# Kernel tuning notes

Measured on AMD Instinct MI355X. Metric: run time of the kernel, lower is better.

Reference implementation:

```python
import jax, jax.numpy as jnp
import numpy as np

B, T = 128, 256
H = 200                      # hidden_dim
EMB, POSD, NERD = 300, 30, 30
VOCAB, NPOS, NNER = 40000, 50, 25
NCLASS = 2
IN = EMB + POSD + NERD


def setup_inputs():
    key = jax.random.key(0)
    ks = jax.random.split(key, 32)
    words = jax.random.randint(ks[0], (B, T), 1, VOCAB)
    lengths = jax.random.randint(ks[1], (B,), T // 2, T + 1)
    t = jnp.arange(T)
    masks = (t[None, :] >= lengths[:, None]).astype(jnp.int64)  # 1 = pad
    pos = jax.random.randint(ks[2], (B, T), 0, NPOS)
    ner = jax.random.randint(ks[3], (B, T), 0, NNER)

    def span_pos(k, span):  # relative position encoding, 0 on entity span
        start = jax.random.randint(k, (B,), 0, T // 2 - span)
        rel = t[None, :] - start[:, None]
        return jnp.where(rel < 0, rel, jnp.where(rel < span, 0, rel - span + 1)).astype(jnp.int64)

    subj_pos = span_pos(ks[4], 3)
    obj_pos = span_pos(ks[5], 2)

    s = 0.08
    def rn(k, shape):
        return jax.random.normal(k, shape, dtype=jnp.float32) * s

    p = {}
    p["emb_w"] = rn(ks[6], (VOCAB, EMB)).at[0].set(0.0)  # PAD row
    p["pos_w"] = rn(ks[7], (NPOS, POSD))
    p["ner_w"] = rn(ks[8], (NNER, NERD))
    dims = [IN, 2 * H]
    i = 9
    for l in range(2):
        for d in ("f", "b"):
            p["w_ih_l%d%s" % (l, d)] = rn(ks[i], (4 * H, dims[l])); i += 1
            p["w_hh_l%d%s" % (l, d)] = rn(ks[i], (4 * H, H)); i += 1
            p["b_l%d%s" % (l, d)] = rn(ks[i], (4 * H,)); i += 1
    p["wo_w"] = rn(ks[i], (H, 2 * H)); p["wo_b"] = rn(ks[i + 1], (H,))
    p["ws_w"] = rn(ks[i + 2], (H, 2 * H)); p["ws_b"] = rn(ks[i + 3], (H,))
    p["wg_w"] = rn(ks[i + 4], (H, 2 * H)); p["wg_b"] = rn(ks[i + 5], (H,))
    p["cls_w"] = rn(ks[i + 6], (NCLASS, H)); p["cls_b"] = rn(ks[i + 7], (NCLASS,))
    return dict(words=words, masks=masks, pos=pos, ner=ner,
                subj_pos=subj_pos, obj_pos=obj_pos, **p)


def lstm_dir(x, keep, w_ih, w_hh, b, reverse):
    """Packed-sequence-equivalent LSTM: state frozen and output zeroed at pads.
    x: [B,T,D], keep: [B,T] (1.0 = real token). Returns ([B,T,H], final h [B,H])."""
    Hh = w_hh.shape[1]

    def step(carry, inp):
        h, c = carry
        xt, mt = inp  # [B,D], [B,1]
        g = xt @ w_ih.T + h @ w_hh.T + b
        i, f, gg, o = jnp.split(g, 4, axis=-1)  # torch gate order i,f,g,o
        cn = jax.nn.sigmoid(f) * c + jax.nn.sigmoid(i) * jnp.tanh(gg)
        hn = jax.nn.sigmoid(o) * jnp.tanh(cn)
        h = mt * hn + (1.0 - mt) * h
        c = mt * cn + (1.0 - mt) * c
        return (h, c), h * mt

    b_ = x.shape[0]
    h0 = jnp.zeros((b_, Hh), x.dtype)
    xs = (jnp.swapaxes(x, 0, 1), keep.T[..., None])
    (hT, _), ys = jax.lax.scan(step, (h0, h0), xs, reverse=reverse)
    return jnp.swapaxes(ys, 0, 1), hT


def attn_pool(q, kv, pad):
    # single-query attention: q [B,D], kv [B,T,D], pad [B,T] bool
    d_k = q.shape[-1]
    scores = jnp.einsum("bd,btd->bt", q, kv) / jnp.sqrt(jnp.float32(d_k))
    scores = jnp.where(pad, jnp.float32(-1e9), scores)
    p = jax.nn.softmax(scores, axis=-1)
    return jnp.einsum("bt,btd->bd", p, kv)


def _forward(words, masks, pos, ner, subj_pos, obj_pos,
             emb_w, pos_w, ner_w,
             w_ih_l0f, w_hh_l0f, b_l0f, w_ih_l0b, w_hh_l0b, b_l0b,
             w_ih_l1f, w_hh_l1f, b_l1f, w_ih_l1b, w_hh_l1b, b_l1b,
             wo_w, wo_b, ws_w, ws_b, wg_w, wg_b, cls_w, cls_b):
    embs = jnp.concatenate([emb_w[words], pos_w[pos], ner_w[ner]], axis=-1)
    keep = (masks == 0).astype(embs.dtype)
    of0, _ = lstm_dir(embs, keep, w_ih_l0f, w_hh_l0f, b_l0f, False)
    ob0, _ = lstm_dir(embs, keep, w_ih_l0b, w_hh_l0b, b_l0b, True)
    x1 = jnp.concatenate([of0, ob0], axis=-1)
    of1, hf1 = lstm_dir(x1, keep, w_ih_l1f, w_hh_l1f, b_l1f, False)
    ob1, hb1 = lstm_dir(x1, keep, w_ih_l1b, w_hh_l1b, b_l1b, True)
    rnn_out = jnp.concatenate([of1, ob1], axis=-1)  # [B,T,2H]

    pad = masks != 0
    # masked gather-sum over entity spans: (rel_pos + mask) == 0 selects span tokens
    subj_sel = ((subj_pos + masks) == 0).astype(rnn_out.dtype)[..., None]
    obj_sel = ((obj_pos + masks) == 0).astype(rnn_out.dtype)[..., None]
    subj_h = jnp.sum(rnn_out * subj_sel, axis=1)  # [B,2H]
    obj_h = jnp.sum(rnn_out * obj_sel, axis=1)
    glob_h = jnp.concatenate([hb1, hf1], axis=-1)  # hidden[-1]=last bwd, hidden[-2]=last fwd

    obj_a = attn_pool(obj_h, rnn_out, pad)
    subj_a = attn_pool(subj_h, rnn_out, pad)
    glob_a = attn_pool(glob_h, rnn_out, pad)

    h = jax.nn.relu(obj_a @ wo_w.T + wo_b + subj_a @ ws_w.T + ws_b + glob_a @ wg_w.T + wg_b)
    return h @ cls_w.T + cls_b  # [B, NCLASS]


def reference(words, masks, pos, ner, subj_pos, obj_pos,
              emb_w, pos_w, ner_w,
              w_ih_l0f, w_hh_l0f, b_l0f, w_ih_l0b, w_hh_l0b, b_l0b,
              w_ih_l1f, w_hh_l1f, b_l1f, w_ih_l1b, w_hh_l1b, b_l1b,
              wo_w, wo_b, ws_w, ws_b, wg_w, wg_b, cls_w, cls_b):
    return _forward(words, masks, pos, ner, subj_pos, obj_pos,
                    emb_w, pos_w, ner_w,
                    w_ih_l0f, w_hh_l0f, b_l0f, w_ih_l0b, w_hh_l0b, b_l0b,
                    w_ih_l1f, w_hh_l1f, b_l1f, w_ih_l1b, w_hh_l1b, b_l1b,
                    wo_w, wo_b, ws_w, ws_b, wg_w, wg_b, cls_w, cls_b)
```

## Files before the change

kernel.cpp:

```cpp
#include <hip/hip_runtime.h>
#include <hip/hip_bf16.h>
#include <math.h>

constexpr int B = 128;
constexpr int T = 256;
constexpr int H = 200;
constexpr int G4 = 800;
constexpr int BT = B * T;
constexpr int K0 = 360, K0P = 384;
constexpr int K1 = 400, K1P = 416;

typedef __bf16 bf16x8 __attribute__((ext_vector_type(8)));
typedef float f32x4 __attribute__((ext_vector_type(4)));
typedef _Float16 half2v __attribute__((ext_vector_type(2)));
typedef unsigned uix4 __attribute__((ext_vector_type(4)));

__device__ __forceinline__ float bfr2f(unsigned short u) {
  union { unsigned int i; float f; } x;
  x.i = ((unsigned int)u) << 16;
  return x.f;
}
__device__ __forceinline__ unsigned short f2hu(float f) {
  _Float16 h = (_Float16)f;
  return *(unsigned short*)&h;
}
__device__ __forceinline__ half2v ash2(unsigned u) {
  union { unsigned v; half2v h; } x;
  x.v = u;
  return x.h;
}
__device__ __forceinline__ float sigm(float x) {
  return 1.0f / (1.0f + __expf(-x));
}
__device__ __forceinline__ float tanh_f(float x) {
  float e = __expf(2.0f * x);
  return (e - 1.0f) / (e + 1.0f);
}
__device__ __forceinline__ float ldraw(const void* p, size_t i, int f) {
  return f ? ((const float*)p)[i] : bfr2f(((const unsigned short*)p)[i]);
}

__global__ void detect_dtype(const unsigned short* __restrict__ raw,
                             int* __restrict__ flag) {
  __shared__ int cnt[256];
  int c = 0;
  for (int j = 0; j < 32; ++j) {
    unsigned short u = raw[1024 + threadIdx.x * 32 + j];
    int e = (u >> 7) & 0xFF;
    if (e >= 0xC0) ++c;
  }
  cnt[threadIdx.x] = c;
  __syncthreads();
  for (int off = 128; off > 0; off >>= 1) {
    if (threadIdx.x < off) cnt[threadIdx.x] += cnt[threadIdx.x + off];
    __syncthreads();
  }
  if (threadIdx.x == 0) *flag = (cnt[0] > 16) ? 1 : 0;
}

__global__ __launch_bounds__(256) void embed_fill(
    const int* __restrict__ words,
    const int* __restrict__ pos,
    const int* __restrict__ ner,
    const void* __restrict__ emb_w,
    const void* __restrict__ pos_w,
    const void* __restrict__ ner_w,
    __hip_bfloat16* __restrict__ X0,
    uix4* __restrict__ z0, size_t n0,
    uix4* __restrict__ z1, size_t n1,
    const int* __restrict__ flag) {
  if (blockIdx.x < 4096) {
    int bt = blockIdx.x * 8 + (threadIdx.x >> 5);
    int j0 = threadIdx.x & 31;
    int f = *flag;
    int w = words[bt], p = pos[bt], nr = ner[bt];
    for (int j = j0; j < K0P; j += 32) {
      float v;
      if (j < 300)       v = ldraw(emb_w, (size_t)w * 300 + j, f);
      else if (j < 330)  v = ldraw(pos_w, (size_t)p * 30 + (j - 300), f);
      else if (j < 360)  v = ldraw(ner_w, (size_t)nr * 30 + (j - 330), f);
      else               v = 0.0f;
      X0[(size_t)bt * K0P + j] = __float2bfloat16(v);
    }
  } else {
    size_t i = (size_t)(blockIdx.x - 4096) * 256 + threadIdx.x;
    size_t stride = (size_t)2048 * 256;
    uix4 z = {0u, 0u, 0u, 0u};
    size_t nt = n0 + n1;
    for (; i < nt; i += stride) {
      if (i < n0) z0[i] = z;
      else        z1[i - n0] = z;
    }
  }
}

__global__ __launch_bounds__(256) void prep_weights(
    const void* __restrict__ whh0, const void* __restrict__ whh1,
    const void* __restrict__ whh2, const void* __restrict__ whh3,
    unsigned* __restrict__ wpack,
    const void* __restrict__ wih0f, const void* __restrict__ wih0b,
    __hip_bfloat16* __restrict__ wih0p,
    const void* __restrict__ wih1f, const void* __restrict__ wih1b,
    __hip_bfloat16* __restrict__ wih1p,
    const int* __restrict__ flag) {
  int blk = blockIdx.x;
  int f = *flag;
  if (blk < 1250) {
    int idx = blk * 256 + threadIdx.x;
    if (idx >= 4 * G4 * 100) return;
    int m = idx / (G4 * 100);
    int loc = idx - m * (G4 * 100);
    const void* src = (m == 0) ? whh0 : (m == 1) ? whh1 : (m == 2) ? whh2 : whh3;
    int n = loc / 100, p = loc - n * 100;
    float lo_f = ldraw(src, (size_t)n * 200 + 2 * p, f);
    float hi_f = ldraw(src, (size_t)n * 200 + 2 * p + 1, f);
    wpack[idx] = (unsigned)f2hu(lo_f) | ((unsigned)f2hu(hi_f) << 16);
  } else if (blk < 2850) {
    int r = blk - 1250;
    const void* src = (r < G4) ? wih0f : wih0b;
    int rr = (r < G4) ? r : r - G4;
    for (int j = threadIdx.x; j < K0P; j += 256) {
      float v = (j < K0) ? ldraw(src, (size_t)rr * K0 + j, f) : 0.0f;
      wih0p[(size_t)r * K0P + j] = __float2bfloat16(v);
    }
  } else {
    int r = blk - 2850;
    const void* src = (r < G4) ? wih1f : wih1b;
    int rr = (r < G4) ? r : r - G4;
    for (int j = threadIdx.x; j < K1P; j += 256) {
      float v = (j < K1) ? ldraw(src, (size_t)rr * K1 + j, f) : 0.0f;
      wih1p[(size_t)r * K1P + j] = __float2bfloat16(v);
    }
  }
}

__global__ __launch_bounds__(256) void gemm_bt(
    const __hip_bfloat16* __restrict__ A,
    const __hip_bfloat16* __restrict__ Bm,
    __hip_bfloat16* __restrict__ C,
    int N, int Kp) {
  const int tid = threadIdx.x;
  const int lane = tid & 63;
  const int wave = tid >> 6;
  const int l15 = lane & 15, quad = lane >> 4;
  const int wr = wave & 1, wc = wave >> 1;

  const int blk = blockIdx.x;
  const int x = blk & 7, j = blk >> 3;
  const int m0 = (x + 8 * (j / 13)) * 128;
  const int n0 = (j % 13) * 128;

  __shared__ __align__(16) __hip_bfloat16 Ab[2][128 * 64];
  __shared__ __align__(16) __hip_bfloat16 Bb[2][128 * 64];

  f32x4 acc[4][4] = {};

  const int nk = (Kp + 63) >> 6;

  uix4 st[8];
  auto stage_issue = [&](int kt) {
    const int k0 = kt << 6;
    #pragma unroll
    for (int jj = 0; jj < 8; ++jj) {
      int c = tid + (jj & 3) * 256;
      int row = c >> 3, p = c & 7;
      int qd = p ^ (row & 7);
      int kcol = k0 + qd * 8;
      uix4 z = {0u, 0u, 0u, 0u};
      if (kcol + 8 <= Kp) {
        if (jj < 4) {
          st[jj] = *(const uix4*)(A + (size_t)(m0 + row) * Kp + kcol);
        } else {
          int br = n0 + row; if (br > N - 1) br = N - 1;
          st[jj] = *(const uix4*)(Bm + (size_t)br * Kp + kcol);
        }
      } else {
        st[jj] = z;
      }
    }
  };
  auto stage_write = [&](int buf) {
    #pragma unroll
    for (int jj = 0; jj < 8; ++jj) {
      int c = tid + (jj & 3) * 256;
      if (jj < 4) *(uix4*)((char*)&Ab[buf][0] + c * 16) = st[jj];
      else        *(uix4*)((char*)&Bb[buf][0] + c * 16) = st[jj];
    }
  };

  stage_issue(0);
  stage_write(0);
  __syncthreads();

  for (int kt = 0; kt < nk; ++kt) {
    const int buf = kt & 1;
    if (kt + 1 < nk) stage_issue(kt + 1);

    #pragma unroll
    for (int k32 = 0; k32 < 2; ++k32) {
      bf16x8 a[4], b[4];
      #pragma unroll
      for (int mi = 0; mi < 4; ++mi) {
        int row = wr * 64 + mi * 16 + l15;
        int p = (k32 * 4 + quad) ^ (row & 7);
        a[mi] = *(const bf16x8*)((const char*)&Ab[buf][0] + (row * 8 + p) * 16);
      }
      #pragma unroll
      for (int ni = 0; ni < 4; ++ni) {
        int row = wc * 64 + ni * 16 + l15;
        int p = (k32 * 4 + quad) ^ (row & 7);
        b[ni] = *(const bf16x8*)((const char*)&Bb[buf][0] + (row * 8 + p) * 16);
      }
      #pragma unroll
      for (int mi = 0; mi < 4; ++mi)
        #pragma unroll
        for (int ni = 0; ni < 4; ++ni)
          acc[mi][ni] = __builtin_amdgcn_mfma_f32_16x16x32_bf16(
              a[mi], b[ni], acc[mi][ni], 0, 0, 0);
    }

    if (kt + 1 < nk) stage_write((kt + 1) & 1);
    __syncthreads();
  }

  #pragma unroll
  for (int mi = 0; mi < 4; ++mi)
    #pragma unroll
    for (int ni = 0; ni < 4; ++ni)
      #pragma unroll
      for (int r = 0; r < 4; ++r) {
        int row = m0 + wr * 64 + mi * 16 + quad * 4 + r;
        int col = n0 + wc * 64 + ni * 16 + l15;
        if (col < N)
          C[(size_t)row * N + col] = __float2bfloat16(acc[mi][ni][r]);
      }
}

__global__ __launch_bounds__(512, 2) void lstm_row(
    const __hip_bfloat16* __restrict__ Gpre,
    const unsigned* __restrict__ Wpack,
    const void* __restrict__ bias_f_raw,
    const void* __restrict__ bias_b_raw,
    const int* __restrict__ masks,
    __hip_bfloat16* __restrict__ out,
    int ostride,
    float* __restrict__ final_h,
    const int* __restrict__ flag)
{
  const int tid = threadIdx.x;
  const int dir = blockIdx.x >> 7;
  const int row = blockIdx.x & 127;
  const int wave = tid >> 6;
  const int lane = tid & 63;
  const int kq = wave & 3;
  const int gs = ((wave >> 2) << 6) | lane;
  const bool tail = (gs >= 96);

  __shared__ __align__(16) _Float16 hsh[256];
  __shared__ float parts[4 * 804];
  __shared__ int lensh[256];
  __shared__ int bigbuf[21504];

  const unsigned* wb = Wpack + (size_t)dir * G4 * 100;

  for (int i = tid; i < 3200; i += 512) {
    int g = i / 100, c = i - g * 100;
    bigbuf[g * 101 + c] = (int)wb[(768 + g) * 100 + c];
  }
  if (tid < 256) lensh[tid] = (masks[row * T + tid] == 0) ? 1 : 0;

  unsigned w[6][25];
  {
    const unsigned* s = wb + gs * 100 + kq * 25;
    #pragma unroll
    for (int j = 0; j < 6; ++j)
      #pragma unroll
      for (int p = 0; p < 25; ++p)
        w[j][p] = s[12800 * j + p];
  }
  const unsigned* wt = (const unsigned*)&bigbuf[(gs - 96) * 101 + kq * 25];

  const int u = tid;
  const int f = *flag;
  const void* braw = dir ? bias_b_raw : bias_f_raw;
  float bI = 0.f, bF = 0.f, bG = 0.f, bO = 0.f;
  if (u < 200) {
    bI = ldraw(braw, u, f);
    bF = ldraw(braw, 200 + u, f);
    bG = ldraw(braw, 400 + u, f);
    bO = ldraw(braw, 600 + u, f);
  }

  if (tid < 256) hsh[tid] = (_Float16)0.0f;
  float creg = 0.0f, hreg = 0.0f;
  __syncthreads();

  for (int off = 128; off > 0; off >>= 1) {
    if (tid < off) lensh[tid] += lensh[tid + off];
    __syncthreads();
  }
  const int len = lensh[0];

  const unsigned short* gp = (const unsigned short*)Gpre + dir * 800;
  const size_t gbase = (size_t)row * T;
  const uix4* hvp = (const uix4*)((const char*)hsh + kq * 128);
  const int hwrite = (u / 50) * 64 + (u % 50);

  #pragma unroll 1
  for (int tt = 0; tt < len; ++tt) {
    const int t = dir ? (len - 1 - tt) : tt;
    const size_t goff = (gbase + t) * 1600;
    unsigned short qI = 0, qF = 0, qG = 0, qO = 0;
    if (u < 200) {
      qI = gp[goff + u];
      qF = gp[goff + 200 + u];
      qG = gp[goff + 400 + u];
      qO = gp[goff + 600 + u];
    }

    uix4 hb[7];
    #pragma unroll
    for (int i = 0; i < 7; ++i) hb[i] = hvp[i];

    float a0 = 0.f, a1 = 0.f, a2 = 0.f, a3 = 0.f, a4 = 0.f, a5 = 0.f;
    #pragma unroll
    for (int p = 0; p < 25; ++p) {
      half2v h2 = ash2(hb[p >> 2][p & 3]);
      a0 = __builtin_amdgcn_fdot2(ash2(w[0][p]), h2, a0, false);
      a1 = __builtin_amdgcn_fdot2(ash2(w[1][p]), h2, a1, false);
      a2 = __builtin_amdgcn_fdot2(ash2(w[2][p]), h2, a2, false);
      a3 = __builtin_amdgcn_fdot2(ash2(w[3][p]), h2, a3, false);
      a4 = __builtin_amdgcn_fdot2(ash2(w[4][p]), h2, a4, false);
      a5 = __builtin_amdgcn_fdot2(ash2(w[5][p]), h2, a5, false);
    }
    const int pb = kq * 804;
    parts[pb + gs]        = a0;
    parts[pb + 128 + gs]  = a1;
    parts[pb + 256 + gs]  = a2;
    parts[pb + 384 + gs]  = a3;
    parts[pb + 512 + gs]  = a4;
    parts[pb + 640 + gs]  = a5;
    if (tail) {
      float a6 = 0.f;
      #pragma unroll
      for (int p = 0; p < 25; ++p)
        a6 = __builtin_amdgcn_fdot2(ash2(wt[p]), ash2(hb[p >> 2][p & 3]), a6, false);
      parts[pb + 672 + gs] = a6;
    }
    __syncthreads();

    if (u < 200) {
      float gi = parts[u]       + parts[804 + u]       + parts[1608 + u]       + parts[2412 + u]       + bI + bfr2f(qI);
      float gf = parts[200 + u] + parts[804 + 200 + u] + parts[1608 + 200 + u] + parts[2412 + 200 + u] + bF + bfr2f(qF);
      float gg = parts[400 + u] + parts[804 + 400 + u] + parts[1608 + 400 + u] + parts[2412 + 400 + u] + bG + bfr2f(qG);
      float go = parts[600 + u] + parts[804 + 600 + u] + parts[1608 + 600 + u] + parts[2412 + 600 + u] + bO + bfr2f(qO);
      float si = sigm(gi), sf = sigm(gf), so = sigm(go);
      float cn = sf * creg + si * tanh_f(gg);
      float hn = so * tanh_f(cn);
      creg = cn;
      hreg = hn;
      hsh[hwrite] = (_Float16)hn;
      out[((size_t)row * T + t) * ostride + dir * H + u] = __float2bfloat16(hn);
    }
    __syncthreads();
  }

  if (final_h != nullptr && u < 200) {
    int col = dir ? u : (H + u);
    final_h[(size_t)row * 400 + col] = hreg;
  }
}

__global__ __launch_bounds__(256) void span_sum(
    const __hip_bfloat16* __restrict__ rnn,
    const int* __restrict__ masks,
    const int* __restrict__ subj_pos,
    const int* __restrict__ obj_pos,
    float* __restrict__ obj_h,
    float* __restrict__ subj_h)
{
  int b = blockIdx.x;
  int tc = threadIdx.x >> 6;
  int dv = threadIdx.x & 63;
  __shared__ float aS[4][400];
  __shared__ float aO[4][400];

  float ss[8] = {}, so[8] = {};
  if (dv < 50) {
    for (int t = tc * 64; t < tc * 64 + 64; ++t) {
      int m = masks[b * T + t];
      int fs = (subj_pos[b * T + t] + m) == 0;
      int fo = (obj_pos[b * T + t] + m) == 0;
      if (fs | fo) {
        uix4 v = *(const uix4*)(rnn + ((size_t)b * T + t) * 400 + dv * 8);
        #pragma unroll
        for (int j = 0; j < 4; ++j) {
          float lo = bfr2f((unsigned short)(v[j] & 0xFFFF));
          float hi = bfr2f((unsigned short)(v[j] >> 16));
          if (fs) { ss[2 * j] += lo; ss[2 * j + 1] += hi; }
          if (fo) { so[2 * j] += lo; so[2 * j + 1] += hi; }
        }
      }
    }
    #pragma unroll
    for (int k = 0; k < 8; ++k) {
      aS[tc][dv * 8 + k] = ss[k];
      aO[tc][dv * 8 + k] = so[k];
    }
  }
  __syncthreads();
  for (int d = threadIdx.x; d < 400; d += 256) {
    subj_h[(size_t)b * 400 + d] = aS[0][d] + aS[1][d] + aS[2][d] + aS[3][d];
    obj_h[(size_t)b * 400 + d]  = aO[0][d] + aO[1][d] + aO[2][d] + aO[3][d];
  }
}

__global__ __launch_bounds__(256) void attn_pool_k(
    const float* __restrict__ qbuf,
    const __hip_bfloat16* __restrict__ rnn,
    const int* __restrict__ masks,
    float* __restrict__ outp)
{
  int b = blockIdx.x & 127;
  int qi = blockIdx.x >> 7;
  __shared__ float qs[400];
  __shared__ float ps[256];
  __shared__ float red[256];
  __shared__ float acc4[4][400];
  const float* q = qbuf + ((size_t)qi * B + b) * 400;
  for (int d = threadIdx.x; d < 400; d += 256) qs[d] = q[d];
  __syncthreads();

  int t = threadIdx.x;
  const uix4* kvv = (const uix4*)(rnn + ((size_t)b * T + t) * 400);
  float s = 0.f;
  #pragma unroll 5
  for (int i = 0; i < 50; ++i) {
    uix4 v = kvv[i];
    #pragma unroll
    for (int j = 0; j < 4; ++j) {
      s += bfr2f((unsigned short)(v[j] & 0xFFFF)) * qs[8 * i + 2 * j];
      s += bfr2f((unsigned short)(v[j] >> 16))    * qs[8 * i + 2 * j + 1];
    }
  }
  s *= 0.05f;
  if (masks[b * T + t] != 0) s = -1e9f;

  red[t] = s;
  __syncthreads();
  for (int off = 128; off > 0; off >>= 1) {
    if (t < off) red[t] = fmaxf(red[t], red[t + off]);
    __syncthreads();
  }
  float mx = red[0];
  __syncthreads();
  float e = expf(s - mx);
  red[t] = e;
  __syncthreads();
  for (int off = 128; off > 0; off >>= 1) {
    if (t < off) red[t] += red[t + off];
    __syncthreads();
  }
  float inv = 1.0f / red[0];
  ps[t] = e * inv;
  __syncthreads();

  int tc = threadIdx.x >> 6;
  int dv = threadIdx.x & 63;
  float a[8] = {};
  if (dv < 50) {
    for (int t2 = tc * 64; t2 < tc * 64 + 64; ++t2) {
      float wgt = ps[t2];
      if (wgt != 0.f) {
        uix4 v = *(const uix4*)(rnn + ((size_t)b * T + t2) * 400 + dv * 8);
        #pragma unroll
        for (int j = 0; j < 4; ++j) {
          a[2 * j]     += wgt * bfr2f((unsigned short)(v[j] & 0xFFFF));
          a[2 * j + 1] += wgt * bfr2f((unsigned short)(v[j] >> 16));
        }
      }
    }
    #pragma unroll
    for (int k = 0; k < 8; ++k) acc4[tc][dv * 8 + k] = a[k];
  }
  __syncthreads();
  for (int d = threadIdx.x; d < 400; d += 256)
    outp[((size_t)qi * B + b) * 400 + d] =
        acc4[0][d] + acc4[1][d] + acc4[2][d] + acc4[3][d];
}

__global__ __launch_bounds__(256) void final_head(
    const float* __restrict__ attn,
    const void* __restrict__ wo_w, const void* __restrict__ wo_b,
    const void* __restrict__ ws_w, const void* __restrict__ ws_b,
    const void* __restrict__ wg_w, const void* __restrict__ wg_b,
    const void* __restrict__ cls_w, const void* __restrict__ cls_b,
    void* __restrict__ outp,
    const int* __restrict__ flag)
{
  int b = blockIdx.x;
  int f = *flag;
  __shared__ float hs[H];
  int j = threadIdx.x;
  if (j < H) {
    float acc = ldraw(wo_b, j, f) + ldraw(ws_b, j, f) + ldraw(wg_b, j, f);
    const float* oa = attn + ((size_t)0 * B + b) * 400;
    const float* sa = attn + ((size_t)1 * B + b) * 400;
    const float* ga = attn + ((size_t)2 * B + b) * 400;
    for (int d = 0; d < 400; ++d) {
      acc += oa[d] * ldraw(wo_w, (size_t)j * 400 + d, f);
      acc += sa[d] * ldraw(ws_w, (size_t)j * 400 + d, f);
      acc += ga[d] * ldraw(wg_w, (size_t)j * 400 + d, f);
    }
    hs[j] = fmaxf(acc, 0.0f);
  }
  __syncthreads();
  if (j < 2) {
    float a = ldraw(cls_b, j, f);
    for (int k = 0; k < H; ++k)
      a += hs[k] * ldraw(cls_w, (size_t)j * H + k, f);
    if (f) ((float*)outp)[b * 2 + j] = a;
    else   ((__hip_bfloat16*)outp)[b * 2 + j] = __float2bfloat16(a);
  }
}

constexpr size_t O_X0   = 0;
constexpr size_t O_X1   = 25165824;
constexpr size_t O_GPRE = 52428800;
constexpr size_t O_RNN  = 157286400;
constexpr size_t O_WIH0 = 183500800;
constexpr size_t O_WIH1 = 184729600;
constexpr size_t O_WPK  = 186060800;
constexpr size_t O_Q    = 187340800;
constexpr size_t O_ATT  = 187955200;
constexpr size_t O_FLAG = 188569600;

extern "C" void kernel_launch(void* const* d_in, const int* in_sizes, int n_in,
                              void* d_out, int out_size, void* d_ws, size_t ws_size,
                              hipStream_t stream) {
  (void)in_sizes; (void)n_in; (void)out_size; (void)ws_size;

  const int* words = (const int*)d_in[0];
  const int* masks = (const int*)d_in[1];
  const int* pos   = (const int*)d_in[2];
  const int* ner   = (const int*)d_in[3];
  const int* subj  = (const int*)d_in[4];
  const int* obj   = (const int*)d_in[5];
  const void* emb_w = d_in[6];
  const void* pos_w = d_in[7];
  const void* ner_w = d_in[8];
  const void* wih[4]  = {d_in[9],  d_in[12], d_in[15], d_in[18]};
  const void* whh[4]  = {d_in[10], d_in[13], d_in[16], d_in[19]};
  const void* bias[4] = {d_in[11], d_in[14], d_in[17], d_in[20]};
  const void* wo_w = d_in[21]; const void* wo_b = d_in[22];
  const void* ws_w = d_in[23]; const void* ws_b = d_in[24];
  const void* wg_w = d_in[25]; const void* wg_b = d_in[26];
  const void* cls_w = d_in[27]; const void* cls_b = d_in[28];

  char* ws = (char*)d_ws;
  __hip_bfloat16* X0   = (__hip_bfloat16*)(ws + O_X0);
  __hip_bfloat16* X1   = (__hip_bfloat16*)(ws + O_X1);
  __hip_bfloat16* Gpre = (__hip_bfloat16*)(ws + O_GPRE);
  __hip_bfloat16* RNN  = (__hip_bfloat16*)(ws + O_RNN);
  __hip_bfloat16* wih0p = (__hip_bfloat16*)(ws + O_WIH0);
  __hip_bfloat16* wih1p = (__hip_bfloat16*)(ws + O_WIH1);
  unsigned* Wpack = (unsigned*)(ws + O_WPK);
  float* qbuf = (float*)(ws + O_Q);
  float* attb = (float*)(ws + O_ATT);
  int* flag = (int*)(ws + O_FLAG);

  detect_dtype<<<1, 256, 0, stream>>>((const unsigned short*)emb_w, flag);
  prep_weights<<<4450, 256, 0, stream>>>(
      whh[0], whh[1], whh[2], whh[3], Wpack,
      wih[0], wih[1], wih0p, wih[2], wih[3], wih1p, flag);

  embed_fill<<<6144, 256, 0, stream>>>(words, pos, ner, emb_w, pos_w, ner_w,
                                       X0,
                                       (uix4*)X1, (size_t)BT * K1P * 2 / 16,
                                       (uix4*)RNN, (size_t)BT * 400 * 2 / 16,
                                       flag);

  const int ggrid = (BT / 128) * 13;

  gemm_bt<<<ggrid, 256, 0, stream>>>(X0, wih0p, Gpre, 1600, K0P);
  lstm_row<<<256, 512, 0, stream>>>(Gpre, Wpack, bias[0], bias[1], masks,
                                    X1, K1P, nullptr, flag);

  gemm_bt<<<ggrid, 256, 0, stream>>>(X1, wih1p, Gpre, 1600, K1P);
  float* qglob = qbuf + (size_t)2 * B * 400;
  lstm_row<<<256, 512, 0, stream>>>(Gpre, Wpack + (size_t)2 * G4 * 100,
                                    bias[2], bias[3], masks,
                                    RNN, 400, qglob, flag);

  span_sum<<<B, 256, 0, stream>>>(RNN, masks, subj, obj,
                                  qbuf, qbuf + (size_t)B * 400);

  attn_pool_k<<<3 * B, 256, 0, stream>>>(qbuf, RNN, masks, attb);

  final_head<<<B, 256, 0, stream>>>(attb, wo_w, wo_b, ws_w, ws_b, wg_w, wg_b,
                                    cls_w, cls_b, d_out, flag);
}
```

Before: 1.119 ms.

## Use direct global-to-LDS loads in GEMM and merge prep kernels

The input-projection GEMM now stages full K tiles with global_load_lds instead of loading into registers and then writing LDS. The loop is restructured so the load for tile kt is issued before compute on tile kt-1, with one barrier per iteration, and a register path is kept only for the partial tail tile. The weight-prep and embedding/zero-fill kernels are also merged into one launch to save a kernel launch. Correctness depends on the async LDS writes being complete at the barrier, and the LSTM recurrence, which dominates runtime, is unchanged.

```diff
diff --git a/kernel.cpp b/kernel.cpp
--- a/kernel.cpp
+++ b/kernel.cpp
@@ -38,6 +38,12 @@
 }
 __device__ __forceinline__ float ldraw(const void* p, size_t i, int f) {
   return f ? ((const float*)p)[i] : bfr2f(((const unsigned short*)p)[i]);
+}
+
+__device__ __forceinline__ void glds16(const void* g, void* l) {
+  __builtin_amdgcn_global_load_lds(
+      (const __attribute__((address_space(1))) unsigned int*)g,
+      (__attribute__((address_space(3))) unsigned int*)l, 16, 0, 0);
 }
 
 __global__ void detect_dtype(const unsigned short* __restrict__ raw,
@@ -58,7 +64,14 @@
   if (threadIdx.x == 0) *flag = (cnt[0] > 16) ? 1 : 0;
 }
 
-__global__ __launch_bounds__(256) void embed_fill(
+__global__ __launch_bounds__(256) void prep_all(
+    const void* __restrict__ whh0, const void* __restrict__ whh1,
+    const void* __restrict__ whh2, const void* __restrict__ whh3,
+    unsigned* __restrict__ wpack,
+    const void* __restrict__ wih0f, const void* __restrict__ wih0b,
+    __hip_bfloat16* __restrict__ wih0p,
+    const void* __restrict__ wih1f, const void* __restrict__ wih1b,
+    __hip_bfloat16* __restrict__ wih1p,
     const int* __restrict__ words,
     const int* __restrict__ pos,
     const int* __restrict__ ner,
@@ -68,40 +81,6 @@
     __hip_bfloat16* __restrict__ X0,
     uix4* __restrict__ z0, size_t n0,
     uix4* __restrict__ z1, size_t n1,
-    const int* __restrict__ flag) {
-  if (blockIdx.x < 4096) {
-    int bt = blockIdx.x * 8 + (threadIdx.x >> 5);
-    int j0 = threadIdx.x & 31;
-    int f = *flag;
-    int w = words[bt], p = pos[bt], nr = ner[bt];
-    for (int j = j0; j < K0P; j += 32) {
-      float v;
-      if (j < 300)       v = ldraw(emb_w, (size_t)w * 300 + j, f);
-      else if (j < 330)  v = ldraw(pos_w, (size_t)p * 30 + (j - 300), f);
-      else if (j < 360)  v = ldraw(ner_w, (size_t)nr * 30 + (j - 330), f);
-      else               v = 0.0f;
-      X0[(size_t)bt * K0P + j] = __float2bfloat16(v);
-    }
-  } else {
-    size_t i = (size_t)(blockIdx.x - 4096) * 256 + threadIdx.x;
-    size_t stride = (size_t)2048 * 256;
-    uix4 z = {0u, 0u, 0u, 0u};
-    size_t nt = n0 + n1;
-    for (; i < nt; i += stride) {
-      if (i < n0) z0[i] = z;
-      else        z1[i - n0] = z;
-    }
-  }
-}
-
-__global__ __launch_bounds__(256) void prep_weights(
-    const void* __restrict__ whh0, const void* __restrict__ whh1,
-    const void* __restrict__ whh2, const void* __restrict__ whh3,
-    unsigned* __restrict__ wpack,
-    const void* __restrict__ wih0f, const void* __restrict__ wih0b,
-    __hip_bfloat16* __restrict__ wih0p,
-    const void* __restrict__ wih1f, const void* __restrict__ wih1b,
-    __hip_bfloat16* __restrict__ wih1p,
     const int* __restrict__ flag) {
   int blk = blockIdx.x;
   int f = *flag;
@@ -123,13 +102,34 @@
       float v = (j < K0) ? ldraw(src, (size_t)rr * K0 + j, f) : 0.0f;
       wih0p[(size_t)r * K0P + j] = __float2bfloat16(v);
     }
-  } else {
+  } else if (blk < 4450) {
     int r = blk - 2850;
     const void* src = (r < G4) ? wih1f : wih1b;
     int rr = (r < G4) ? r : r - G4;
     for (int j = threadIdx.x; j < K1P; j += 256) {
       float v = (j < K1) ? ldraw(src, (size_t)rr * K1 + j, f) : 0.0f;
       wih1p[(size_t)r * K1P + j] = __float2bfloat16(v);
+    }
+  } else if (blk < 8546) {
+    int bt = (blk - 4450) * 8 + (threadIdx.x >> 5);
+    int j0 = threadIdx.x & 31;
+    int w = words[bt], p = pos[bt], nr = ner[bt];
+    for (int j = j0; j < K0P; j += 32) {
+      float v;
+      if (j < 300)       v = ldraw(emb_w, (size_t)w * 300 + j, f);
+      else if (j < 330)  v = ldraw(pos_w, (size_t)p * 30 + (j - 300), f);
+      else if (j < 360)  v = ldraw(ner_w, (size_t)nr * 30 + (j - 330), f);
+      else               v = 0.0f;
+      X0[(size_t)bt * K0P + j] = __float2bfloat16(v);
+    }
+  } else {
+    size_t i = (size_t)(blk - 8546) * 256 + threadIdx.x;
+    size_t stride = (size_t)2048 * 256;
+    uix4 z = {0u, 0u, 0u, 0u};
+    size_t nt = n0 + n1;
+    for (; i < nt; i += stride) {
+      if (i < n0) z0[i] = z;
+      else        z1[i - n0] = z;
     }
   }
 }
@@ -155,71 +155,74 @@
 
   f32x4 acc[4][4] = {};
 
-  const int nk = (Kp + 63) >> 6;
-
-  uix4 st[8];
-  auto stage_issue = [&](int kt) {
-    const int k0 = kt << 6;
-    #pragma unroll
-    for (int jj = 0; jj < 8; ++jj) {
-      int c = tid + (jj & 3) * 256;
-      int row = c >> 3, p = c & 7;
-      int qd = p ^ (row & 7);
-      int kcol = k0 + qd * 8;
-      uix4 z = {0u, 0u, 0u, 0u};
-      if (kcol + 8 <= Kp) {
-        if (jj < 4) {
-          st[jj] = *(const uix4*)(A + (size_t)(m0 + row) * Kp + kcol);
-        } else {
+  const int nk_full = Kp >> 6;
+  const int nk = nk_full + ((Kp & 63) ? 1 : 0);
+
+  for (int kt = 0; kt <= nk; ++kt) {
+    if (kt < nk) {
+      const int buf = kt & 1;
+      if (kt < nk_full) {
+        const int k0 = kt << 6;
+        #pragma unroll
+        for (int jj = 0; jj < 4; ++jj) {
+          int c = tid + jj * 256;
+          int row = c >> 3, p = c & 7;
+          int qd = p ^ (row & 7);
+          glds16(A + (size_t)(m0 + row) * Kp + k0 + qd * 8,
+                 (char*)&Ab[buf][0] + c * 16);
           int br = n0 + row; if (br > N - 1) br = N - 1;
-          st[jj] = *(const uix4*)(Bm + (size_t)br * Kp + kcol);
+          glds16(Bm + (size_t)br * Kp + k0 + qd * 8,
+                 (char*)&Bb[buf][0] + c * 16);
         }
       } else {
-        st[jj] = z;
+        const int k0 = nk_full << 6;
+        #pragma unroll
+        for (int jj = 0; jj < 8; ++jj) {
+          int c = tid + (jj & 3) * 256;
+          int row = c >> 3, p = c & 7;
+          int qd = p ^ (row & 7);
+          int kcol = k0 + qd * 8;
+          uix4 v = {0u, 0u, 0u, 0u};
+          if (kcol + 8 <= Kp) {
+            if (jj < 4) {
+              v = *(const uix4*)(A + (size_t)(m0 + row) * Kp + kcol);
+            } else {
+              int br = n0 + row; if (br > N - 1) br = N - 1;
+              v = *(const uix4*)(Bm + (size_t)br * Kp + kcol);
+            }
+          }
+          if (jj < 4) *(uix4*)((char*)&Ab[buf][0] + c * 16) = v;
+          else        *(uix4*)((char*)&Bb[buf][0] + c * 16) = v;
+        }
       }
     }
-  };
-  auto stage_write = [&](int buf) {
-    #pragma unroll
-    for (int jj = 0; jj < 8; ++jj) {
-      int c = tid + (jj & 3) * 256;
-      if (jj < 4) *(uix4*)((char*)&Ab[buf][0] + c * 16) = st[jj];
-      else        *(uix4*)((char*)&Bb[buf][0] + c * 16) = st[jj];
-    }
-  };
-
-  stage_issue(0);
-  stage_write(0);
-  __syncthreads();
-
-  for (int kt = 0; kt < nk; ++kt) {
-    const int buf = kt & 1;
-    if (kt + 1 < nk) stage_issue(kt + 1);
-
-    #pragma unroll
-    for (int k32 = 0; k32 < 2; ++k32) {
-      bf16x8 a[4], b[4];
+
+    if (kt > 0) {
+      const int buf = (kt - 1) & 1;
       #pragma unroll
-      for (int mi = 0; mi < 4; ++mi) {
-        int row = wr * 64 + mi * 16 + l15;
-        int p = (k32 * 4 + quad) ^ (row & 7);
-        a[mi] = *(const bf16x8*)((const char*)&Ab[buf][0] + (row * 8 + p) * 16);
+      for (int k32 = 0; k32 < 2; ++k32) {
+        bf16x8 a[4], b[4];
+        #pragma unroll
+        for (int mi = 0; mi < 4; ++mi) {
+          int row = wr * 64 + mi * 16 + l15;
+          int p = (k32 * 4 + quad) ^ (row & 7);
+          a[mi] = *(const bf16x8*)((const char*)&Ab[buf][0] + (row * 8 + p) * 16);
+        }
+        #pragma unroll
+        for (int ni = 0; ni < 4; ++ni) {
+          int row = wc * 64 + ni * 16 + l15;
+          int p = (k32 * 4 + quad) ^ (row & 7);
+          b[ni] = *(const bf16x8*)((const char*)&Bb[buf][0] + (row * 8 + p) * 16);
+        }
+        #pragma unroll
+        for (int mi = 0; mi < 4; ++mi)
+          #pragma unroll
+          for (int ni = 0; ni < 4; ++ni)
+            acc[mi][ni] = __builtin_amdgcn_mfma_f32_16x16x32_bf16(
+                a[mi], b[ni], acc[mi][ni], 0, 0, 0);
       }
-      #pragma unroll
-      for (int ni = 0; ni < 4; ++ni) {
-        int row = wc * 64 + ni * 16 + l15;
-        int p = (k32 * 4 + quad) ^ (row & 7);
-        b[ni] = *(const bf16x8*)((const char*)&Bb[buf][0] + (row * 8 + p) * 16);
-      }
-      #pragma unroll
-      for (int mi = 0; mi < 4; ++mi)
-        #pragma unroll
-        for (int ni = 0; ni < 4; ++ni)
-          acc[mi][ni] = __builtin_amdgcn_mfma_f32_16x16x32_bf16(
-              a[mi], b[ni], acc[mi][ni], 0, 0, 0);
-    }
-
-    if (kt + 1 < nk) stage_write((kt + 1) & 1);
+    }
+
     __syncthreads();
   }
 
@@ -570,15 +573,13 @@
   int* flag = (int*)(ws + O_FLAG);
 
   detect_dtype<<<1, 256, 0, stream>>>((const unsigned short*)emb_w, flag);
-  prep_weights<<<4450, 256, 0, stream>>>(
+  prep_all<<<10594, 256, 0, stream>>>(
       whh[0], whh[1], whh[2], whh[3], Wpack,
-      wih[0], wih[1], wih0p, wih[2], wih[3], wih1p, flag);
-
-  embed_fill<<<6144, 256, 0, stream>>>(words, pos, ner, emb_w, pos_w, ner_w,
-                                       X0,
-                                       (uix4*)X1, (size_t)BT * K1P * 2 / 16,
-                                       (uix4*)RNN, (size_t)BT * 400 * 2 / 16,
-                                       flag);
+      wih[0], wih[1], wih0p, wih[2], wih[3], wih1p,
+      words, pos, ner, emb_w, pos_w, ner_w, X0,
+      (uix4*)X1, (size_t)BT * K1P * 2 / 16,
+      (uix4*)RNN, (size_t)BT * 400 * 2 / 16,
+      flag);
 
   const int ggrid = (BT / 128) * 13;
 
```

Result: no change. 1.116 ms (-0.3%).
